# Optimization experiments

Hardware: AMD Instinct MI355X
Metric: run time of the kernel (lower is better)

Reference implementation:

```python
import jax, jax.numpy as jnp
import numpy as np

B, S, D, H, R = 4, 1024, 1024, 16, 4
HD = D // H
EPS = 1e-5


def layer_norm(x, g, b):
    mu = jnp.mean(x, axis=-1, keepdims=True)
    var = jnp.mean(jnp.square(x - mu), axis=-1, keepdims=True)
    return (x - mu) * jax.lax.rsqrt(var + EPS) * g + b


def setup_inputs() -> dict:
    key = jax.random.key(0)
    ks = jax.random.split(key, 12)
    sd = 1.0 / np.sqrt(D)
    sf = 1.0 / np.sqrt(R * D)
    inp = {
        "x": jax.random.normal(ks[0], (B, S, D), jnp.float32),
        "ln1_g": jnp.ones((D,), jnp.float32),
        "ln1_b": jnp.zeros((D,), jnp.float32),
        "wq": jax.random.uniform(ks[1], (D, D), jnp.float32, -sd, sd),
        "bq": jnp.zeros((D,), jnp.float32),
        "wk": jax.random.uniform(ks[2], (D, D), jnp.float32, -sd, sd),
        "bk": jnp.zeros((D,), jnp.float32),
        "wv": jax.random.uniform(ks[3], (D, D), jnp.float32, -sd, sd),
        "bv": jnp.zeros((D,), jnp.float32),
        "wo": jax.random.uniform(ks[4], (D, D), jnp.float32, -sd, sd),
        "bo": jnp.zeros((D,), jnp.float32),
        "ln2_g": jnp.ones((D,), jnp.float32),
        "ln2_b": jnp.zeros((D,), jnp.float32),
        "w1": jax.random.uniform(ks[5], (D, R * D), jnp.float32, -sd, sd),
        "b1": jnp.zeros((R * D,), jnp.float32),
        "w2": jax.random.uniform(ks[6], (R * D, D), jnp.float32, -sf, sf),
        "b2": jnp.zeros((D,), jnp.float32),
    }
    return inp


def reference(x, ln1_g, ln1_b, wq, bq, wk, bk, wv, bv, wo, bo,
              ln2_g, ln2_b, w1, b1, w2, b2):
    # Pre-LN MHA. Per-head Q/K/V linears concatenated == one batched projection
    # reshaped into heads, so we batch all heads in single GEMMs.
    h = layer_norm(x, ln1_g, ln1_b)
    q = (h @ wq + bq).reshape(B, S, H, HD)
    k = (h @ wk + bk).reshape(B, S, H, HD)
    v = (h @ wv + bv).reshape(B, S, H, HD)
    scores = jnp.einsum("bqhd,bkhd->bhqk", q, k) / np.sqrt(HD)
    attn = jax.nn.softmax(scores, axis=-1)
    ctx = jnp.einsum("bhqk,bkhd->bqhd", attn, v).reshape(B, S, D)
    x = x + ctx @ wo + bo
    # Pre-LN MLP with exact (erf) GELU, matching torch nn.GELU default.
    h2 = layer_norm(x, ln2_g, ln2_b)
    mlp = jax.nn.gelu(h2 @ w1 + b1, approximate=False) @ w2 + b2
    return x + mlp
```

## Files before the change

kernel.cpp:

```cpp
#include <hip/hip_runtime.h>

typedef unsigned short u16;
typedef __attribute__((ext_vector_type(8))) __bf16 bf16x8;
typedef __attribute__((ext_vector_type(4))) float floatx4;

#define FLAG_F32OUT  1
#define FLAG_GELU    2
#define FLAG_PARTIAL 4
#define FLAG_PBF16   8

__device__ __forceinline__ u16 f2bf(float f) {
  union { float f; unsigned u; } un;
  un.f = f;
  unsigned u = un.u;
  u += 0x7fffu + ((u >> 16) & 1u);
  return (u16)(u >> 16);
}

__device__ __forceinline__ float bf2f(u16 h) {
  union { unsigned u; float f; } un;
  un.u = ((unsigned)h) << 16;
  return un.f;
}

__device__ __forceinline__ float gelu_f(float x) {
  float t = 1.5957691216f * (x + 0.044715f * x * x * x);
  return x / (1.0f + __expf(-t));
}

__device__ __forceinline__ floatx4 mfma16(bf16x8 a, bf16x8 b, floatx4 c) {
  return __builtin_amdgcn_mfma_f32_16x16x32_bf16(a, b, c, 0, 0, 0);
}

__device__ __forceinline__ void glds16(const void* g, void* l) {
  __builtin_amdgcn_global_load_lds(
      (__attribute__((address_space(1))) unsigned int*)(void*)g,
      (__attribute__((address_space(3))) unsigned int*)l, 16, 0, 0);
}

__global__ __launch_bounds__(256) void prep_all(
    const float* __restrict__ wq, const float* __restrict__ wk,
    const float* __restrict__ wv, const float* __restrict__ wo,
    const float* __restrict__ w1, const float* __restrict__ w2,
    const float* __restrict__ bq, const float* __restrict__ bk,
    const float* __restrict__ bv,
    u16* __restrict__ wqkvt, u16* __restrict__ wot,
    u16* __restrict__ w1t, u16* __restrict__ w2t,
    float* __restrict__ bqkv,
    const float* __restrict__ x, const float* __restrict__ ln1g,
    const float* __restrict__ ln1b, u16* __restrict__ h) {
  int b = blockIdx.x;
  int tx = threadIdx.x, ty = threadIdx.y;
  int tid = ty * 32 + tx;
  if (b >= 12300) {
    int row = b - 12300;
    const float4* xr = (const float4*)(x + (size_t)row * 1024);
    float4 v = xr[tid];
    float s = v.x + v.y + v.z + v.w;
    float s2 = v.x * v.x + v.y * v.y + v.z * v.z + v.w * v.w;
#pragma unroll
    for (int m = 32; m >= 1; m >>= 1) {
      s += __shfl_xor(s, m, 64);
      s2 += __shfl_xor(s2, m, 64);
    }
    __shared__ float red[8];
    int wave = tid >> 6, lane = tid & 63;
    if (lane == 0) { red[wave] = s; red[4 + wave] = s2; }
    __syncthreads();
    s = red[0] + red[1] + red[2] + red[3];
    s2 = red[4] + red[5] + red[6] + red[7];
    float mu = s * (1.0f / 1024.0f);
    float var = s2 * (1.0f / 1024.0f) - mu * mu;
    float inv = rsqrtf(var + 1e-5f);
    float4 gv = ((const float4*)ln1g)[tid];
    float4 bv2 = ((const float4*)ln1b)[tid];
    ushort4 ov;
    ov.x = f2bf((v.x - mu) * inv * gv.x + bv2.x);
    ov.y = f2bf((v.y - mu) * inv * gv.y + bv2.y);
    ov.z = f2bf((v.z - mu) * inv * gv.z + bv2.z);
    ov.w = f2bf((v.w - mu) * inv * gv.w + bv2.w);
    *(ushort4*)(h + (size_t)row * 1024 + tid * 4) = ov;
    return;
  }
  if (b >= 12288) {
    int i = (b - 12288) * 256 + tid;
    float v = (i < 1024) ? bq[i] * 0.125f
                         : (i < 2048 ? bk[i - 1024] : bv[i - 2048]);
    bqkv[i] = v;
    return;
  }
  const float* W;
  u16* Wt;
  int K, N, bx, by;
  float scale = 1.0f;
  if (b < 4096) {
    int w = b >> 10, t = b & 1023;
    bx = t & 31; by = t >> 5; K = 1024; N = 1024;
    if (w == 0)      { W = wq; Wt = wqkvt;                scale = 0.125f; }
    else if (w == 1) { W = wk; Wt = wqkvt + 1024 * 1024; }
    else if (w == 2) { W = wv; Wt = wqkvt + 2 * 1024 * 1024; }
    else             { W = wo; Wt = wot; }
  } else if (b < 8192) {
    int t = b - 4096;
    bx = t & 127; by = t >> 7; K = 1024; N = 4096; W = w1; Wt = w1t;
  } else {
    int t = b - 8192;
    bx = t & 31; by = t >> 5; K = 4096; N = 1024; W = w2; Wt = w2t;
  }
  __shared__ float tile[32][33];
  int n0 = bx * 32, k0 = by * 32;
#pragma unroll
  for (int i = 0; i < 4; ++i)
    tile[ty + i * 8][tx] = W[(size_t)(k0 + ty + i * 8) * N + n0 + tx];
  __syncthreads();
#pragma unroll
  for (int i = 0; i < 4; ++i)
    Wt[(size_t)(n0 + ty + i * 8) * K + k0 + tx] =
        f2bf(tile[tx][ty + i * 8] * scale);
}

__global__ __launch_bounds__(256, 4) void gemm_bt(
    const u16* __restrict__ A, const u16* __restrict__ Bt,
    const float* __restrict__ bias,
    void* __restrict__ outp, void* __restrict__ outp2,
    int M, int N, int K, int Ks, int flags) {
  __shared__ __align__(16) u16 smem[17408];
  u16* As = smem;
  u16* Bs = smem + 8192;
  int tid = threadIdx.x;
  int lane = tid & 63, wave = tid >> 6;
  int lm = lane & 15, quad = lane >> 4;
  int wm = (wave >> 1) * 64, wn = (wave & 1) * 64;
  int bm = blockIdx.x, bn = blockIdx.y;
  int koff = blockIdx.z * Ks;

  const u16* aP = A + (size_t)(bm * 128 + (tid >> 2)) * K + koff + (tid & 3) * 8;
  const u16* bP = Bt + (size_t)(bn * 128 + (tid >> 2)) * K + koff + (tid & 3) * 8;
  u16* asD = As + tid * 8;
  u16* bsD = Bs + tid * 8;
  size_t rstep = (size_t)64 * K;

  floatx4 acc[4][4];
#pragma unroll
  for (int i = 0; i < 4; ++i)
#pragma unroll
    for (int j = 0; j < 4; ++j) acc[i][j] = (floatx4){0.f, 0.f, 0.f, 0.f};

  for (int k0 = 0; k0 < Ks; k0 += 64) {
#pragma unroll
    for (int p = 0; p < 2; ++p) {
      glds16(aP + p * 32, asD + p * 4096);
      glds16(aP + p * 32 + rstep, asD + p * 4096 + 2048);
      glds16(bP + p * 32, bsD + p * 4096);
      glds16(bP + p * 32 + rstep, bsD + p * 4096 + 2048);
    }
    aP += 64;
    bP += 64;
    __syncthreads();
#pragma unroll
    for (int p = 0; p < 2; ++p) {
      bf16x8 af[4], bfr[4];
#pragma unroll
      for (int mi = 0; mi < 4; ++mi)
        af[mi] = *(const bf16x8*)&As[p * 4096 + (wm + mi * 16 + lm) * 32 + quad * 8];
#pragma unroll
      for (int ni = 0; ni < 4; ++ni)
        bfr[ni] = *(const bf16x8*)&Bs[p * 4096 + (wn + ni * 16 + lm) * 32 + quad * 8];
#pragma unroll
      for (int mi = 0; mi < 4; ++mi)
#pragma unroll
        for (int ni = 0; ni < 4; ++ni)
          acc[mi][ni] = mfma16(af[mi], bfr[ni], acc[mi][ni]);
    }
    __syncthreads();
  }

  bool gelu = (flags & FLAG_GELU) != 0;
  bool part = (flags & FLAG_PARTIAL) != 0;
  bool pbf = (flags & FLAG_PBF16) != 0;
  bool f32p = ((flags & FLAG_F32OUT) != 0) ||
              (part && !(pbf && blockIdx.z > 0));
  void* op;
  if (blockIdx.z == 0)
    op = outp;
  else
    op = (char*)outp2 +
         (size_t)(blockIdx.z - 1) * M * N * (pbf ? 2 : 4);

  if (!f32p) {
    u16* Ct = smem;
#pragma unroll
    for (int ni = 0; ni < 4; ++ni) {
      int col = bn * 128 + wn + ni * 16 + lm;
      float bv = part ? 0.0f : bias[col];
#pragma unroll
      for (int mi = 0; mi < 4; ++mi) {
        int lr0 = wm + mi * 16 + quad * 4;
#pragma unroll
        for (int r = 0; r < 4; ++r) {
          float vv = acc[mi][ni][r] + bv;
          if (gelu) vv = gelu_f(vv);
          Ct[(lr0 + r) * 136 + wn + ni * 16 + lm] = f2bf(vv);
        }
      }
    }
    __syncthreads();
#pragma unroll
    for (int p = 0; p < 8; ++p) {
      int unit = p * 256 + tid;
      int row = unit >> 4, ch = unit & 15;
      uint4 v = *(const uint4*)&Ct[row * 136 + ch * 8];
      *(uint4*)&((u16*)op)[(size_t)(bm * 128 + row) * N + bn * 128 + ch * 8] = v;
    }
  } else {
    float* Cf = (float*)smem;
#pragma unroll
    for (int pp = 0; pp < 2; ++pp) {
      __syncthreads();
      if ((wave >> 1) == pp) {
#pragma unroll
        for (int ni = 0; ni < 4; ++ni) {
          int col = bn * 128 + wn + ni * 16 + lm;
          float bv = part ? 0.0f : bias[col];
#pragma unroll
          for (int mi = 0; mi < 4; ++mi) {
            int lr0 = mi * 16 + quad * 4;
#pragma unroll
            for (int r = 0; r < 4; ++r) {
              float vv = acc[mi][ni][r] + bv;
              if (gelu) vv = gelu_f(vv);
              Cf[(lr0 + r) * 132 + wn + ni * 16 + lm] = vv;
            }
          }
        }
      }
      __syncthreads();
#pragma unroll
      for (int p = 0; p < 8; ++p) {
        int unit = p * 256 + tid;
        int row = unit >> 5, ch = unit & 31;
        float4 v = *(const float4*)&Cf[row * 132 + ch * 4];
        size_t gi = (size_t)(bm * 128 + pp * 64 + row) * N + bn * 128 + ch * 4;
        *(float4*)&((float*)op)[gi] = v;
      }
    }
  }
}

__global__ __launch_bounds__(512) void flash_attn(
    const u16* __restrict__ qkv, u16* __restrict__ ctx) {
  __shared__ __align__(16) u16 Qs[128 * 72];
  __shared__ __align__(16) u16 Ks[2][64 * 72];
  __shared__ __align__(16) u16 Vt[2][64 * 64];

  int tid = threadIdx.x;
  int lane = tid & 63, wave = tid >> 6;
  int lm = lane & 15, quad = lane >> 4;
  int qt = blockIdx.x & 7;
  int hh = (blockIdx.x >> 3) & 15;
  int b = blockIdx.x >> 7;

  int krow = tid >> 3;
  int col8 = (tid & 7) * 8;
  int cb = col8 >> 3;

  size_t base_q = ((size_t)(b * 1024 + qt * 128)) * 3072 + hh * 64;
#pragma unroll
  for (int r = 0; r < 2; ++r) {
    int idx = r * 512 + tid;
    int row = idx >> 3;
    int c8 = (idx & 7) * 8;
    *(uint4*)&Qs[row * 72 + c8] =
        *(const uint4*)&qkv[base_q + (size_t)row * 3072 + c8];
  }
  __syncthreads();
  bf16x8 a0 = *(const bf16x8*)&Qs[(wave * 16 + lm) * 72 + quad * 8];
  bf16x8 a1 = *(const bf16x8*)&Qs[(wave * 16 + lm) * 72 + 32 + quad * 8];
  u16* Ps = &Qs[wave * 16 * 72];

  float l_r[4];
  floatx4 acc[4];
#pragma unroll
  for (int r = 0; r < 4; ++r) l_r[r] = 0.0f;
#pragma unroll
  for (int d = 0; d < 4; ++d) acc[d] = (floatx4){0.f, 0.f, 0.f, 0.f};

  size_t kv0 = ((size_t)(b * 1024 + krow)) * 3072 + 1024 + hh * 64 + col8;
  const size_t kv_step = (size_t)64 * 3072;

  uint4 kreg = *(const uint4*)&qkv[kv0];
  uint4 vreg = *(const uint4*)&qkv[kv0 + 1024];

  int rw = krow >> 3;
  int rl = krow & 7;

  for (int j = 0; j < 16; ++j) {
    u16* KsB = Ks[j & 1];
    u16* VtB = Vt[j & 1];
    *(uint4*)&KsB[krow * 72 + col8] = kreg;
    {
      u16* ve = (u16*)&vreg;
#pragma unroll
      for (int e = 0; e < 8; ++e) {
        int d = col8 + e;
        int chunk = (rw ^ cb ^ e) & 7;
        VtB[d * 64 + chunk * 8 + rl] = ve[e];
      }
    }
    if (j < 15) {
      size_t kvn = kv0 + (size_t)(j + 1) * kv_step;
      kreg = *(const uint4*)&qkv[kvn];
      vreg = *(const uint4*)&qkv[kvn + 1024];
    }
    __syncthreads();

    floatx4 sacc[4];
#pragma unroll
    for (int ni = 0; ni < 4; ++ni) {
      bf16x8 b0 = *(const bf16x8*)&KsB[(ni * 16 + lm) * 72 + quad * 8];
      bf16x8 b1 = *(const bf16x8*)&KsB[(ni * 16 + lm) * 72 + 32 + quad * 8];
      floatx4 z = (floatx4){0.f, 0.f, 0.f, 0.f};
      z = mfma16(a0, b0, z);
      z = mfma16(a1, b1, z);
      sacc[ni] = z;
    }

#pragma unroll
    for (int r = 0; r < 4; ++r) {
      float p0 = __expf(sacc[0][r]);
      float p1 = __expf(sacc[1][r]);
      float p2 = __expf(sacc[2][r]);
      float p3 = __expf(sacc[3][r]);
      l_r[r] += (p0 + p1) + (p2 + p3);
      Ps[(quad * 4 + r) * 72 + 0 * 16 + lm] = f2bf(p0);
      Ps[(quad * 4 + r) * 72 + 1 * 16 + lm] = f2bf(p1);
      Ps[(quad * 4 + r) * 72 + 2 * 16 + lm] = f2bf(p2);
      Ps[(quad * 4 + r) * 72 + 3 * 16 + lm] = f2bf(p3);
    }

    bf16x8 pa0 = *(const bf16x8*)&Ps[lm * 72 + quad * 8];
    bf16x8 pa1 = *(const bf16x8*)&Ps[lm * 72 + 32 + quad * 8];
#pragma unroll
    for (int dd = 0; dd < 4; ++dd) {
      int d = dd * 16 + lm;
      int dx = ((d >> 3) ^ d) & 7;
      bf16x8 vb0 = *(const bf16x8*)&VtB[d * 64 + ((quad ^ dx) & 7) * 8];
      bf16x8 vb1 = *(const bf16x8*)&VtB[d * 64 + (((4 + quad) ^ dx) & 7) * 8];
      acc[dd] = mfma16(pa0, vb0, acc[dd]);
      acc[dd] = mfma16(pa1, vb1, acc[dd]);
    }
  }

  float rl4[4];
#pragma unroll
  for (int r = 0; r < 4; ++r) {
    float sm = l_r[r];
#pragma unroll
    for (int mm = 1; mm < 16; mm <<= 1) sm += __shfl_xor(sm, mm, 64);
    rl4[r] = 1.0f / sm;
  }
#pragma unroll
  for (int dd = 0; dd < 4; ++dd)
#pragma unroll
    for (int r = 0; r < 4; ++r)
      Ps[(quad * 4 + r) * 72 + dd * 16 + lm] = f2bf(acc[dd][r] * rl4[r]);
  size_t obase = (size_t)(b * 1024 + qt * 128 + wave * 16);
#pragma unroll
  for (int p = 0; p < 2; ++p) {
    int unit = p * 64 + lane;
    int row = unit >> 3, ch = unit & 7;
    uint4 v = *(const uint4*)&Ps[row * 72 + ch * 8];
    *(uint4*)&ctx[(obase + row) * 1024 + hh * 64 + ch * 8] = v;
  }
}

__global__ __launch_bounds__(256) void reduce_ln(
    float* __restrict__ x2, const float* __restrict__ p1,
    const float* __restrict__ x, const float* __restrict__ bo,
    const float* __restrict__ g, const float* __restrict__ bb,
    u16* __restrict__ h2) {
  int row = blockIdx.x, tid = threadIdx.x;
  size_t base = (size_t)row * 256;
  float4 a = ((const float4*)x2)[base + tid];
  float4 p = ((const float4*)p1)[base + tid];
  float4 c = ((const float4*)x)[base + tid];
  float4 d = ((const float4*)bo)[tid];
  float4 o;
  o.x = a.x + p.x + c.x + d.x;
  o.y = a.y + p.y + c.y + d.y;
  o.z = a.z + p.z + c.z + d.z;
  o.w = a.w + p.w + c.w + d.w;
  ((float4*)x2)[base + tid] = o;

  float s = o.x + o.y + o.z + o.w;
  float s2 = o.x * o.x + o.y * o.y + o.z * o.z + o.w * o.w;
#pragma unroll
  for (int m = 32; m >= 1; m >>= 1) {
    s += __shfl_xor(s, m, 64);
    s2 += __shfl_xor(s2, m, 64);
  }
  __shared__ float red[8];
  int wave = tid >> 6, lane = tid & 63;
  if (lane == 0) { red[wave] = s; red[4 + wave] = s2; }
  __syncthreads();
  s = red[0] + red[1] + red[2] + red[3];
  s2 = red[4] + red[5] + red[6] + red[7];
  float mu = s * (1.0f / 1024.0f);
  float var = s2 * (1.0f / 1024.0f) - mu * mu;
  float inv = rsqrtf(var + 1e-5f);
  float4 gv = ((const float4*)g)[tid];
  float4 bv = ((const float4*)bb)[tid];
  ushort4 ov;
  ov.x = f2bf((o.x - mu) * inv * gv.x + bv.x);
  ov.y = f2bf((o.y - mu) * inv * gv.y + bv.y);
  ov.z = f2bf((o.z - mu) * inv * gv.z + bv.z);
  ov.w = f2bf((o.w - mu) * inv * gv.w + bv.w);
  *(ushort4*)(h2 + (size_t)row * 1024 + tid * 4) = ov;
}

__global__ __launch_bounds__(256) void reduce4b(
    float* __restrict__ out, const u16* __restrict__ pb,
    const float* __restrict__ resid, const float* __restrict__ bias) {
  int i = blockIdx.x * 256 + threadIdx.x;
  float4 a = ((const float4*)out)[i];
  ushort4 q0 = ((const ushort4*)pb)[i];
  ushort4 q1 = ((const ushort4*)(pb + 4194304))[i];
  ushort4 q2 = ((const ushort4*)(pb + 8388608))[i];
  float4 c = ((const float4*)resid)[i];
  float4 d = ((const float4*)bias)[i & 255];
  float4 o;
  o.x = a.x + bf2f(q0.x) + bf2f(q1.x) + bf2f(q2.x) + c.x + d.x;
  o.y = a.y + bf2f(q0.y) + bf2f(q1.y) + bf2f(q2.y) + c.y + d.y;
  o.z = a.z + bf2f(q0.z) + bf2f(q1.z) + bf2f(q2.z) + c.z + d.z;
  o.w = a.w + bf2f(q0.w) + bf2f(q1.w) + bf2f(q2.w) + c.w + d.w;
  ((float4*)out)[i] = o;
}

extern "C" void kernel_launch(void* const* d_in, const int* in_sizes, int n_in,
                              void* d_out, int out_size, void* d_ws, size_t ws_size,
                              hipStream_t stream) {
  const float* x    = (const float*)d_in[0];
  const float* ln1g = (const float*)d_in[1];
  const float* ln1b = (const float*)d_in[2];
  const float* wq   = (const float*)d_in[3];
  const float* bq   = (const float*)d_in[4];
  const float* wk   = (const float*)d_in[5];
  const float* bk   = (const float*)d_in[6];
  const float* wv   = (const float*)d_in[7];
  const float* bv   = (const float*)d_in[8];
  const float* wo   = (const float*)d_in[9];
  const float* bo   = (const float*)d_in[10];
  const float* ln2g = (const float*)d_in[11];
  const float* ln2b = (const float*)d_in[12];
  const float* w1   = (const float*)d_in[13];
  const float* b1   = (const float*)d_in[14];
  const float* w2   = (const float*)d_in[15];
  const float* b2   = (const float*)d_in[16];

  char* ws = (char*)d_ws;
  const size_t MB = 1024ull * 1024ull;
  u16*   h     = (u16*)(ws + 0 * MB);
  u16*   h2    = (u16*)(ws + 0 * MB);
  u16*   qkv   = (u16*)(ws + 8 * MB);
  float* pwo   = (float*)(ws + 8 * MB);
  u16*   act   = (u16*)(ws + 8 * MB);
  u16*   ctxb  = (u16*)(ws + 32 * MB);
  float* bqkv  = (float*)(ws + 32 * MB);
  float* x2    = (float*)(ws + 40 * MB);
  u16*   pw2   = (u16*)(ws + 56 * MB);
  u16*   wqkvt = (u16*)(ws + 64 * MB);
  u16*   wot   = (u16*)(ws + 70 * MB);
  u16*   w1t   = (u16*)(ws + 72 * MB);
  u16*   w2t   = (u16*)(ws + 80 * MB);

  prep_all<<<16396, dim3(32, 8), 0, stream>>>(
      wq, wk, wv, wo, w1, w2, bq, bk, bv, wqkvt, wot, w1t, w2t, bqkv,
      x, ln1g, ln1b, h);

  gemm_bt<<<dim3(32, 24, 1), 256, 0, stream>>>(
      h, wqkvt, bqkv, (void*)qkv, nullptr, 4096, 3072, 1024, 1024, 0);

  flash_attn<<<512, 512, 0, stream>>>(qkv, ctxb);

  gemm_bt<<<dim3(32, 8, 2), 256, 0, stream>>>(
      ctxb, wot, nullptr, (void*)x2, (void*)pwo, 4096, 1024, 1024, 512,
      FLAG_PARTIAL);
  reduce_ln<<<4096, 256, 0, stream>>>(x2, pwo, x, bo, ln2g, ln2b, h2);

  gemm_bt<<<dim3(32, 32, 1), 256, 0, stream>>>(
      h2, w1t, b1, (void*)act, nullptr, 4096, 4096, 1024, 1024, FLAG_GELU);

  gemm_bt<<<dim3(32, 8, 4), 256, 0, stream>>>(
      act, w2t, nullptr, d_out, (void*)pw2, 4096, 1024, 4096, 1024,
      FLAG_PARTIAL | FLAG_PBF16);
  reduce4b<<<4096, 256, 0, stream>>>((float*)d_out, pw2, x2, b2);
}
```

Before: 328.1 us.

## Add 256x128 tile GEMM for MLP layers and single-buffer attention K/V

Adds a gemm_bt2 kernel with 512 threads computing 256x128 output tiles, so each B tile loaded into shared memory is reused across twice as many rows. The two MLP GEMMs now use it, with half as many blocks. The epilogue writes the tile out in halves or quarters through shared memory. Separately, flash attention drops its double-buffered K/V shared-memory tiles for a single buffer with an extra barrier, cutting LDS use in exchange for less overlap.

```diff
diff --git a/kernel.cpp b/kernel.cpp
--- a/kernel.cpp
+++ b/kernel.cpp
@@ -184,8 +184,7 @@
   if (blockIdx.z == 0)
     op = outp;
   else
-    op = (char*)outp2 +
-         (size_t)(blockIdx.z - 1) * M * N * (pbf ? 2 : 4);
+    op = (char*)outp2 + (size_t)(blockIdx.z - 1) * M * N * (pbf ? 2 : 4);
 
   if (!f32p) {
     u16* Ct = smem;
@@ -247,11 +246,144 @@
   }
 }
 
+__global__ __launch_bounds__(512) void gemm_bt2(
+    const u16* __restrict__ A, const u16* __restrict__ Bt,
+    const float* __restrict__ bias,
+    void* __restrict__ outp, void* __restrict__ outp2,
+    int M, int N, int K, int Ks, int flags) {
+  __shared__ __align__(16) u16 smem[24576];
+  u16* As = smem;
+  u16* Bs = smem + 16384;
+  int tid = threadIdx.x;
+  int lane = tid & 63, wave = tid >> 6;
+  int lm = lane & 15, quad = lane >> 4;
+  int wm = (wave & 3) * 64, wn = (wave >> 2) * 64;
+  int bm = blockIdx.x, bn = blockIdx.y;
+  int koff = blockIdx.z * Ks;
+
+  const u16* aP = A + (size_t)(bm * 256 + (tid >> 2)) * K + koff + (tid & 3) * 8;
+  const u16* bP = Bt + (size_t)(bn * 128 + (tid >> 2)) * K + koff + (tid & 3) * 8;
+  u16* asD = As + tid * 8;
+  u16* bsD = Bs + tid * 8;
+  size_t rstepA = (size_t)128 * K;
+
+  floatx4 acc[4][4];
+#pragma unroll
+  for (int i = 0; i < 4; ++i)
+#pragma unroll
+    for (int j = 0; j < 4; ++j) acc[i][j] = (floatx4){0.f, 0.f, 0.f, 0.f};
+
+  for (int k0 = 0; k0 < Ks; k0 += 64) {
+#pragma unroll
+    for (int p = 0; p < 2; ++p) {
+      glds16(aP + p * 32, asD + p * 8192);
+      glds16(aP + p * 32 + rstepA, asD + p * 8192 + 4096);
+      glds16(bP + p * 32, bsD + p * 4096);
+    }
+    aP += 64;
+    bP += 64;
+    __syncthreads();
+#pragma unroll
+    for (int p = 0; p < 2; ++p) {
+      bf16x8 af[4], bfr[4];
+#pragma unroll
+      for (int mi = 0; mi < 4; ++mi)
+        af[mi] = *(const bf16x8*)&As[p * 8192 + (wm + mi * 16 + lm) * 32 + quad * 8];
+#pragma unroll
+      for (int ni = 0; ni < 4; ++ni)
+        bfr[ni] = *(const bf16x8*)&Bs[p * 4096 + (wn + ni * 16 + lm) * 32 + quad * 8];
+#pragma unroll
+      for (int mi = 0; mi < 4; ++mi)
+#pragma unroll
+        for (int ni = 0; ni < 4; ++ni)
+          acc[mi][ni] = mfma16(af[mi], bfr[ni], acc[mi][ni]);
+    }
+    __syncthreads();
+  }
+
+  bool gelu = (flags & FLAG_GELU) != 0;
+  bool part = (flags & FLAG_PARTIAL) != 0;
+  bool pbf = (flags & FLAG_PBF16) != 0;
+  bool f32p = ((flags & FLAG_F32OUT) != 0) ||
+              (part && !(pbf && blockIdx.z > 0));
+  void* op;
+  if (blockIdx.z == 0)
+    op = outp;
+  else
+    op = (char*)outp2 + (size_t)(blockIdx.z - 1) * M * N * (pbf ? 2 : 4);
+
+  if (!f32p) {
+    u16* Ct = smem;
+#pragma unroll
+    for (int half = 0; half < 2; ++half) {
+      __syncthreads();
+      if ((wm >> 7) == half) {
+#pragma unroll
+        for (int ni = 0; ni < 4; ++ni) {
+          int col = bn * 128 + wn + ni * 16 + lm;
+          float bv = part ? 0.0f : bias[col];
+#pragma unroll
+          for (int mi = 0; mi < 4; ++mi) {
+            int lr0 = (wm & 127) + mi * 16 + quad * 4;
+#pragma unroll
+            for (int r = 0; r < 4; ++r) {
+              float vv = acc[mi][ni][r] + bv;
+              if (gelu) vv = gelu_f(vv);
+              Ct[(lr0 + r) * 136 + wn + ni * 16 + lm] = f2bf(vv);
+            }
+          }
+        }
+      }
+      __syncthreads();
+#pragma unroll
+      for (int p = 0; p < 4; ++p) {
+        int unit = p * 512 + tid;
+        int row = unit >> 4, ch = unit & 15;
+        uint4 v = *(const uint4*)&Ct[row * 136 + ch * 8];
+        *(uint4*)&((u16*)op)[(size_t)(bm * 256 + half * 128 + row) * N +
+                             bn * 128 + ch * 8] = v;
+      }
+    }
+  } else {
+    float* Cf = (float*)smem;
+#pragma unroll
+    for (int q = 0; q < 4; ++q) {
+      __syncthreads();
+      if ((wm >> 6) == q) {
+#pragma unroll
+        for (int ni = 0; ni < 4; ++ni) {
+          int col = bn * 128 + wn + ni * 16 + lm;
+          float bv = part ? 0.0f : bias[col];
+#pragma unroll
+          for (int mi = 0; mi < 4; ++mi) {
+            int lr0 = mi * 16 + quad * 4;
+#pragma unroll
+            for (int r = 0; r < 4; ++r) {
+              float vv = acc[mi][ni][r] + bv;
+              if (gelu) vv = gelu_f(vv);
+              Cf[(lr0 + r) * 132 + wn + ni * 16 + lm] = vv;
+            }
+          }
+        }
+      }
+      __syncthreads();
+#pragma unroll
+      for (int p = 0; p < 4; ++p) {
+        int unit = p * 512 + tid;
+        int row = unit >> 5, ch = unit & 31;
+        float4 v = *(const float4*)&Cf[row * 132 + ch * 4];
+        size_t gi = (size_t)(bm * 256 + q * 64 + row) * N + bn * 128 + ch * 4;
+        *(float4*)&((float*)op)[gi] = v;
+      }
+    }
+  }
+}
+
 __global__ __launch_bounds__(512) void flash_attn(
     const u16* __restrict__ qkv, u16* __restrict__ ctx) {
   __shared__ __align__(16) u16 Qs[128 * 72];
-  __shared__ __align__(16) u16 Ks[2][64 * 72];
-  __shared__ __align__(16) u16 Vt[2][64 * 64];
+  __shared__ __align__(16) u16 Ks[64 * 72];
+  __shared__ __align__(16) u16 Vt[64 * 64];
 
   int tid = threadIdx.x;
   int lane = tid & 63, wave = tid >> 6;
@@ -295,30 +427,30 @@
   int rl = krow & 7;
 
   for (int j = 0; j < 16; ++j) {
-    u16* KsB = Ks[j & 1];
-    u16* VtB = Vt[j & 1];
-    *(uint4*)&KsB[krow * 72 + col8] = kreg;
+    __syncthreads();
+    *(uint4*)&Ks[krow * 72 + col8] = kreg;
     {
       u16* ve = (u16*)&vreg;
 #pragma unroll
       for (int e = 0; e < 8; ++e) {
         int d = col8 + e;
         int chunk = (rw ^ cb ^ e) & 7;
-        VtB[d * 64 + chunk * 8 + rl] = ve[e];
-      }
-    }
+        Vt[d * 64 + chunk * 8 + rl] = ve[e];
+      }
+    }
+    __syncthreads();
+
     if (j < 15) {
       size_t kvn = kv0 + (size_t)(j + 1) * kv_step;
       kreg = *(const uint4*)&qkv[kvn];
       vreg = *(const uint4*)&qkv[kvn + 1024];
     }
-    __syncthreads();
 
     floatx4 sacc[4];
 #pragma unroll
     for (int ni = 0; ni < 4; ++ni) {
-      bf16x8 b0 = *(const bf16x8*)&KsB[(ni * 16 + lm) * 72 + quad * 8];
-      bf16x8 b1 = *(const bf16x8*)&KsB[(ni * 16 + lm) * 72 + 32 + quad * 8];
+      bf16x8 b0 = *(const bf16x8*)&Ks[(ni * 16 + lm) * 72 + quad * 8];
+      bf16x8 b1 = *(const bf16x8*)&Ks[(ni * 16 + lm) * 72 + 32 + quad * 8];
       floatx4 z = (floatx4){0.f, 0.f, 0.f, 0.f};
       z = mfma16(a0, b0, z);
       z = mfma16(a1, b1, z);
@@ -344,8 +476,8 @@
     for (int dd = 0; dd < 4; ++dd) {
       int d = dd * 16 + lm;
       int dx = ((d >> 3) ^ d) & 7;
-      bf16x8 vb0 = *(const bf16x8*)&VtB[d * 64 + ((quad ^ dx) & 7) * 8];
-      bf16x8 vb1 = *(const bf16x8*)&VtB[d * 64 + (((4 + quad) ^ dx) & 7) * 8];
+      bf16x8 vb0 = *(const bf16x8*)&Vt[d * 64 + ((quad ^ dx) & 7) * 8];
+      bf16x8 vb1 = *(const bf16x8*)&Vt[d * 64 + (((4 + quad) ^ dx) & 7) * 8];
       acc[dd] = mfma16(pa0, vb0, acc[dd]);
       acc[dd] = mfma16(pa1, vb1, acc[dd]);
     }
@@ -487,10 +619,10 @@
       FLAG_PARTIAL);
   reduce_ln<<<4096, 256, 0, stream>>>(x2, pwo, x, bo, ln2g, ln2b, h2);
 
-  gemm_bt<<<dim3(32, 32, 1), 256, 0, stream>>>(
+  gemm_bt2<<<dim3(16, 32, 1), 512, 0, stream>>>(
       h2, w1t, b1, (void*)act, nullptr, 4096, 4096, 1024, 1024, FLAG_GELU);
 
-  gemm_bt<<<dim3(32, 8, 4), 256, 0, stream>>>(
+  gemm_bt2<<<dim3(16, 8, 4), 512, 0, stream>>>(
       act, w2t, nullptr, d_out, (void*)pw2, 4096, 1024, 4096, 1024,
       FLAG_PARTIAL | FLAG_PBF16);
   reduce4b<<<4096, 256, 0, stream>>>((float*)d_out, pw2, x2, b2);
```

Result: no change. 330.2 us (+0.6%).
